# Kernel tuning notes

Hardware: AMD Instinct MI355X
Metric: run time of the kernel (lower is better)

## Reference

```python
import jax, jax.numpy as jnp
import numpy as np

# Model hyperparameters (match init_kwargs)
S = 1000        # num_simulations
D = 16          # num_lca_dim
T = 3000        # num_time_steps
THRESHOLD = 1.0
LEAK = 0.1
COMPETITION = 0.1
SELF_EXC = 0.0
NOISE = 1.0
DT = 0.01
SQRT_STEP = float(np.sqrt(0.001))  # LCALayer hardcodes sqrt(0.001) regardless of time_step_size


def setup_inputs() -> dict:
    key = jax.random.key(0)
    ff_input = jax.random.normal(key, (S, D), dtype=jnp.float32)
    return {"ff_input": ff_input}


def reference(ff_input):
    eye = jnp.eye(D, dtype=ff_input.dtype)
    # gamma: off-diagonal = competition, diagonal = -self_excitation
    gamma = COMPETITION * (1.0 - eye) - SELF_EXC * eye
    keys = jax.random.split(jax.random.key(42), T)

    def step(carry, k):
        pre, act = carry
        # accumulators stop integrating once any unit crosses threshold
        active = jnp.all(jnp.abs(act) < THRESHOLD, axis=1, keepdims=True).astype(pre.dtype)
        pre = pre + (ff_input - LEAK * pre - act @ gamma) * active * DT
        dw = jax.random.normal(k, act.shape, dtype=pre.dtype) * (active * NOISE)
        pre = pre + dw * SQRT_STEP
        act = jax.nn.relu(pre)
        return (pre, act), (pre, act)

    init = (jnp.zeros((S, D), jnp.float32), jnp.zeros((S, D), jnp.float32))
    _, (pre_seq, act_seq) = jax.lax.scan(step, init, keys)  # [T, S, D]

    z = jnp.zeros((S, D, 1), jnp.float32)
    pre_all = jnp.concatenate([z, jnp.transpose(pre_seq, (1, 2, 0))], axis=2)  # [S, D, T+1]
    act_all = jnp.concatenate([z, jnp.transpose(act_seq, (1, 2, 0))], axis=2)  # [S, D, T+1]
    return pre_all, act_all
```

## Files before the change

### kernel.cpp

```cpp
#include <hip/hip_runtime.h>
#include <cstdint>

#define T_STEPS 3000
#define S_SIMS  1000
#define D_DIM   16
#define NJ      (S_SIMS * D_DIM)
#define ROW     (T_STEPS + 1)
#define HALF_OUT ((long long)NJ * ROW)

#define NSIMB  250
#define NPROD  7
#define DEPTH  32
#define BATCH  8
#define PAD_FLOATS 13000
#define SQSTEP 0.03162277660168379f

__device__ float g_ws_pre[(size_t)T_STEPS * NJ];

__device__ __forceinline__ uint32_t rotl32(uint32_t v, uint32_t d) {
  return (v << d) | (v >> (32u - d));
}
__device__ __forceinline__ void threefry2x32(uint32_t k0, uint32_t k1,
                                             uint32_t& x0, uint32_t& x1) {
  uint32_t k2 = k0 ^ k1 ^ 0x1BD11BDAu;
  x0 += k0; x1 += k1;
#define TFR(r) { x0 += x1; x1 = rotl32(x1, r); x1 ^= x0; }
  TFR(13u) TFR(15u) TFR(26u) TFR(6u)
  x0 += k1; x1 += k2 + 1u;
  TFR(17u) TFR(29u) TFR(16u) TFR(24u)
  x0 += k2; x1 += k0 + 2u;
  TFR(13u) TFR(15u) TFR(26u) TFR(6u)
  x0 += k0; x1 += k1 + 3u;
  TFR(17u) TFR(29u) TFR(16u) TFR(24u)
  x0 += k1; x1 += k2 + 4u;
  TFR(13u) TFR(15u) TFR(26u) TFR(6u)
  x0 += k2; x1 += k0 + 5u;
#undef TFR
}

__device__ __forceinline__ float bits_to_normal(uint32_t bits) {
  uint32_t fb = (bits >> 9) | 0x3f800000u;
  float f = __uint_as_float(fb) - 1.0f;
  const float lo = -0.99999994f;
  float u = f * 2.0f + lo;
  u = fmaxf(lo, u);
  float w = -0.6931471805599453f * __log2f((1.0f - u) * (1.0f + u));
  float p;
  if (w < 5.0f) {
    w = w - 2.5f;
    p = 2.81022636e-08f;
    p = fmaf(p, w, 3.43273939e-07f);
    p = fmaf(p, w, -3.5233877e-06f);
    p = fmaf(p, w, -4.39150654e-06f);
    p = fmaf(p, w, 0.00021858087f);
    p = fmaf(p, w, -0.00125372503f);
    p = fmaf(p, w, -0.00417768164f);
    p = fmaf(p, w, 0.246640727f);
    p = fmaf(p, w, 1.50140941f);
  } else {
    w = sqrtf(w) - 3.0f;
    p = -0.000200214257f;
    p = fmaf(p, w, 0.000100950558f);
    p = fmaf(p, w, 0.00134934322f);
    p = fmaf(p, w, -0.00367342844f);
    p = fmaf(p, w, 0.00573950773f);
    p = fmaf(p, w, -0.0076224613f);
    p = fmaf(p, w, 0.00943887047f);
    p = fmaf(p, w, 1.00167406f);
    p = fmaf(p, w, 2.83297682f);
  }
  return 1.41421356237f * (p * u);
}

template <int CTRL>
__device__ __forceinline__ float dpp_movf(float v) {
  return __int_as_float(
      __builtin_amdgcn_update_dpp(0, __float_as_int(v), CTRL, 0xF, 0xF, true));
}
__device__ __forceinline__ float row16_sum(float a) {
  float s = a;
  s += dpp_movf<0xB1>(s);
  s += dpp_movf<0x4E>(s);
  s += dpp_movf<0x124>(s);
  s += dpp_movf<0x128>(s);
  return s;
}
__device__ __forceinline__ float row16_max(float a) {
  float m = a;
  m = fmaxf(m, dpp_movf<0xB1>(m));
  m = fmaxf(m, dpp_movf<0x4E>(m));
  m = fmaxf(m, dpp_movf<0x124>(m));
  m = fmaxf(m, dpp_movf<0x128>(m));
  return m;
}

__global__ __launch_bounds__(512) void lca_kernel(const float* __restrict__ ff,
                                                  float* __restrict__ out) {
  __shared__ uint2 sh_keys[T_STEPS];
  __shared__ float sh_nbuf[DEPTH][64];
  __shared__ float sh_pad[PAD_FLOATS];
  __shared__ volatile unsigned sh_prodc[NPROD];
  __shared__ volatile unsigned sh_cons;
  __shared__ volatile unsigned sh_done;
  __shared__ int sh_tf[4];

  const int tid  = threadIdx.x;
  const int lane = tid & 63;
  const int wid  = tid >> 6;
  const int j    = blockIdx.x * 64 + lane;

  for (int i = tid; i < T_STEPS; i += 512) {
    uint32_t x0 = 0u, x1 = (uint32_t)i;
    threefry2x32(0u, 42u, x0, x1);
    sh_keys[i] = make_uint2(x0, x1);
  }
  { volatile float* vp = sh_pad; vp[tid] = 0.0f; }
  if (tid < NPROD) sh_prodc[tid] = 0u;
  if (tid == 0) { sh_cons = 0u; sh_done = 0u; }
  __syncthreads();

  if (wid == 0) {
    __builtin_amdgcn_s_setprio(1);
    const float ffv = ff[j];
    float pre = 0.0f, act = 0.0f;
    bool dead = false;
    int my_tf = T_STEPS;
    unsigned Rc = 0;

#define ENSURE(x)                                                     \
    while (Rc <= (unsigned)(x)) {                                     \
      unsigned mn = 0xffffffffu;                                      \
      for (int p_ = 0; p_ < NPROD; ++p_) {                            \
        unsigned lim = (unsigned)p_ + (unsigned)NPROD * sh_prodc[p_]; \
        if (lim < mn) mn = lim;                                       \
      }                                                               \
      Rc = mn;                                                        \
      if (Rc <= (unsigned)(x)) __builtin_amdgcn_s_sleep(2);           \
    }

    float n[BATCH], nn[BATCH], a[BATCH];
    ENSURE(BATCH - 1);
#pragma unroll
    for (int k = 0; k < BATCH; ++k) n[k] = sh_nbuf[k][lane];

    int t0 = 0;
    while (true) {
      if (lane == 0) sh_cons = (unsigned)(t0 + BATCH);
      const bool more = (t0 + BATCH < T_STEPS);
      if (more) {
        ENSURE(t0 + 2 * BATCH - 1);
#pragma unroll
        for (int k = 0; k < BATCH; ++k)
          nn[k] = sh_nbuf[(t0 + BATCH + k) & (DEPTH - 1)][lane];
      }

      float bmax = 0.0f;
      float* __restrict__ wsp = g_ws_pre + (size_t)t0 * NJ + j;
#pragma unroll
      for (int k = 0; k < BATCH; ++k) {
        float s  = row16_sum(act);
        float e1 = fmaf(-0.1f, pre, ffv);
        float e2 = fmaf(-0.1f, s - act, e1);
        pre = fmaf(e2, 0.01f, pre);
        pre = fmaf(n[k], SQSTEP, pre);
        act = fmaxf(pre, 0.0f);
        a[k] = act;
        bmax = fmaxf(bmax, act);
        if (!dead) wsp[(size_t)k * NJ] = pre;
      }

      if (__any(bmax >= 1.0f)) {
        bool found = dead;
        int ctf = 0;
#pragma unroll
        for (int k = 0; k < BATCH; ++k) {
          float m = row16_max(a[k]);
          if (!found && m >= 1.0f) { found = true; ctf = t0 + k + 1; }
        }
        if (found && !dead) {
          dead = true;
          my_tf = ctf;
          pre = -1e30f;
          act = 0.0f;
        }
        if (__all(dead)) break;
      }

      if (!more) break;
#pragma unroll
      for (int k = 0; k < BATCH; ++k) n[k] = nn[k];
      t0 += BATCH;
    }
#undef ENSURE
    if ((lane & 15) == 0) sh_tf[lane >> 4] = my_tf;
    if (lane == 0) sh_done = 1u;
    __builtin_amdgcn_s_setprio(0);
  } else {
    const int p = wid - 1;
    unsigned count = 0;
    bool quit = false;
    for (int t = p; t < T_STEPS; t += NPROD) {
      if (sh_done) break;
      uint2 k = sh_keys[t];
      uint32_t x0 = 0u, x1 = (uint32_t)j;
      threefry2x32(k.x, k.y, x0, x1);
      float nv = bits_to_normal(x0 ^ x1);
      if (t >= DEPTH) {
        while (true) {
          if (sh_done) { quit = true; break; }
          unsigned pc = sh_cons;
          if ((unsigned)t <= pc + (DEPTH - 1)) break;
          __builtin_amdgcn_s_sleep(4);
        }
        if (quit) break;
      }
      sh_nbuf[t & (DEPTH - 1)][lane] = nv;
      asm volatile("s_waitcnt lgkmcnt(0)" ::: "memory");
      ++count;
      if (lane == 0) sh_prodc[p] = count;
    }
  }

  __syncthreads();

  const int r0 = wid * 8;
#pragma unroll 1
  for (int r = 0; r < 8; ++r) {
    const int jr = blockIdx.x * 64 + r0 + r;
    const int tf = sh_tf[(r0 + r) >> 4];
    float* __restrict__ pre_out = out + (size_t)jr * ROW;
    float* __restrict__ act_out = pre_out + HALF_OUT;
    const float vlast = g_ws_pre[(size_t)(tf - 1) * NJ + jr];
    for (int idx = lane; idx <= tf; idx += 64) {
      float v = (idx == 0) ? 0.0f : g_ws_pre[(size_t)(idx - 1) * NJ + jr];
      pre_out[idx] = v;
      act_out[idx] = fmaxf(v, 0.0f);
    }
    const float va = fmaxf(vlast, 0.0f);
    for (int idx = tf + 1 + lane; idx <= T_STEPS; idx += 64) {
      pre_out[idx] = vlast;
      act_out[idx] = va;
    }
  }
}

extern "C" void kernel_launch(void* const* d_in, const int* in_sizes, int n_in,
                              void* d_out, int out_size, void* d_ws, size_t ws_size,
                              hipStream_t stream) {
  const float* ff = (const float*)d_in[0];
  float* out = (float*)d_out;

  lca_kernel<<<dim3(NSIMB), dim3(512), 0, stream>>>(ff, out);
}
```

Baseline: 106.6 us.

## Transpose workspace through shared-memory tiles and write output with vector stores

The output epilogue used to read the time-major workspace with a per-row strided gather and write one float at a time. It now stages 64x64 tiles in shared memory, reusing the key buffer with padding, so global reads are coalesced. Each row segment is then written with 4-wide vector stores, and the post-threshold tail is filled with vectorized constant stores. This adds extra barriers per tile and relies on 4-byte-aligned vector stores at row offsets that are not 16-byte aligned.

```diff
diff --git a/kernel.cpp b/kernel.cpp
--- a/kernel.cpp
+++ b/kernel.cpp
@@ -14,6 +14,9 @@
 #define BATCH  8
 #define PAD_FLOATS 13000
 #define SQSTEP 0.03162277660168379f
+
+typedef float v4f __attribute__((ext_vector_type(4)));
+typedef v4f uv4f __attribute__((aligned(4)));
 
 __device__ float g_ws_pre[(size_t)T_STEPS * NJ];
 
@@ -99,6 +102,7 @@
   __shared__ uint2 sh_keys[T_STEPS];
   __shared__ float sh_nbuf[DEPTH][64];
   __shared__ float sh_pad[PAD_FLOATS];
+  __shared__ float sh_vlast[64];
   __shared__ volatile unsigned sh_prodc[NPROD];
   __shared__ volatile unsigned sh_cons;
   __shared__ volatile unsigned sh_done;
@@ -107,7 +111,8 @@
   const int tid  = threadIdx.x;
   const int lane = tid & 63;
   const int wid  = tid >> 6;
-  const int j    = blockIdx.x * 64 + lane;
+  const int jb   = blockIdx.x * 64;
+  const int j    = jb + lane;
 
   for (int i = tid; i < T_STEPS; i += 512) {
     uint32_t x0 = 0u, x1 = (uint32_t)i;
@@ -223,25 +228,86 @@
 
   __syncthreads();
 
-  const int r0 = wid * 8;
-#pragma unroll 1
-  for (int r = 0; r < 8; ++r) {
-    const int jr = blockIdx.x * 64 + r0 + r;
-    const int tf = sh_tf[(r0 + r) >> 4];
-    float* __restrict__ pre_out = out + (size_t)jr * ROW;
-    float* __restrict__ act_out = pre_out + HALF_OUT;
-    const float vlast = g_ws_pre[(size_t)(tf - 1) * NJ + jr];
-    for (int idx = lane; idx <= tf; idx += 64) {
-      float v = (idx == 0) ? 0.0f : g_ws_pre[(size_t)(idx - 1) * NJ + jr];
-      pre_out[idx] = v;
-      act_out[idx] = fmaxf(v, 0.0f);
-    }
-    const float va = fmaxf(vlast, 0.0f);
-    for (int idx = tf + 1 + lane; idx <= T_STEPS; idx += 64) {
-      pre_out[idx] = vlast;
-      act_out[idx] = va;
-    }
-  }
+  if (tid < 64) {
+    int tfr = sh_tf[tid >> 4];
+    sh_vlast[tid] = g_ws_pre[(size_t)(tfr - 1) * NJ + jb + tid];
+    float* po = out + (size_t)(jb + tid) * ROW;
+    po[0] = 0.0f;
+    po[HALF_OUT] = 0.0f;
+  }
+  const int maxtf = max(max(sh_tf[0], sh_tf[1]), max(sh_tf[2], sh_tf[3]));
+  float* sh_tilef = (float*)sh_keys;
+#define TILE(tl, r) sh_tilef[(tl) * 65 + (r)]
+
+  const float* __restrict__ wsb = g_ws_pre + jb;
+  for (int tt0 = 0; tt0 < maxtf; tt0 += 64) {
+    __syncthreads();
+#pragma unroll
+    for (int q = 0; q < 8; ++q) {
+      int t = tt0 + wid * 8 + q;
+      float v = 0.0f;
+      if (t < T_STEPS) v = wsb[(size_t)t * NJ + lane];
+      TILE(wid * 8 + q, lane) = v;
+    }
+    __syncthreads();
+#pragma unroll
+    for (int pass = 0; pass < 2; ++pass) {
+      const int r   = wid * 8 + pass * 4 + (lane >> 4);
+      const int tq  = lane & 15;
+      const int jr  = jb + r;
+      const int tfr = sh_tf[r >> 4];
+      const float vl = sh_vlast[r];
+      const int idx = tt0 + 1 + 4 * tq;
+      uv4f vv, av;
+#pragma unroll
+      for (int i = 0; i < 4; ++i) {
+        float tv = TILE(4 * tq + i, r);
+        float v  = (idx + i <= tfr) ? tv : vl;
+        vv[i] = v;
+        av[i] = fmaxf(v, 0.0f);
+      }
+      float* po = out + (size_t)jr * ROW;
+      float* ao = po + HALF_OUT;
+      if (idx + 3 <= T_STEPS) {
+        *(uv4f*)(po + idx) = vv;
+        *(uv4f*)(ao + idx) = av;
+      } else {
+#pragma unroll
+        for (int i = 0; i < 4; ++i)
+          if (idx + i <= T_STEPS) { po[idx + i] = vv[i]; ao[idx + i] = av[i]; }
+      }
+    }
+  }
+
+  const int idxB = (((maxtf + 63) >> 6) << 6) + 1;
+  if (idxB <= T_STEPS) {
+    const int span  = T_STEPS - idxB + 1;
+    const int nquad = span >> 2;
+    const int rem   = span & 3;
+    const int rem_start = idxB + (nquad << 2);
+#pragma unroll
+    for (int pass = 0; pass < 2; ++pass) {
+      const int r  = wid * 8 + pass * 4 + (lane >> 4);
+      const int jr = jb + r;
+      const float vl = sh_vlast[r];
+      const float va = fmaxf(vl, 0.0f);
+      uv4f pv = {vl, vl, vl, vl};
+      uv4f av = {va, va, va, va};
+      float* po = out + (size_t)jr * ROW;
+      float* ao = po + HALF_OUT;
+      for (int qi = (lane & 15); qi < nquad; qi += 16) {
+        const int idx = idxB + 4 * qi;
+        *(uv4f*)(po + idx) = pv;
+        *(uv4f*)(ao + idx) = av;
+      }
+      if ((lane & 15) < rem) {
+        const int idx = rem_start + (lane & 15);
+        po[idx] = vl;
+        ao[idx] = va;
+      }
+    }
+  }
+#undef TILE
 }
 
 extern "C" void kernel_launch(void* const* d_in, const int* in_sizes, int n_in,
```

After: 132.7 us. 1.25x slower.
